# Kernel tuning notes

Hardware: AMD Instinct MI355X
Metric: run time of the kernel (lower is better)

## Reference

```python
import jax, jax.numpy as jnp
import numpy as np
import math

NUM_BITS = 8
EPS = 1e-5


def fake_quant(x, num_bits=NUM_BITS):
    """Uniform fake quantization over the tensor's full range (min/max), STE-friendly."""
    qmax = 2.0 ** num_bits - 1.0
    mn = jnp.min(x)
    mx = jnp.max(x)
    scale = jnp.maximum((mx - mn) / qmax, 1e-8)
    q = jnp.round(jnp.clip((x - mn) / scale, 0.0, qmax)) * scale + mn
    # straight-through estimator: forward = q, backward = identity
    return x + jax.lax.stop_gradient(q - x)


def qconv(x, w, stride, pad):
    """QConv2d: fake-quantize input (8b) and weight (8b), then fp conv (no bias)."""
    return jax.lax.conv_general_dilated(
        fake_quant(x), fake_quant(w),
        window_strides=(stride, stride),
        padding=[(pad, pad), (pad, pad)],
        dimension_numbers=("NCHW", "OIHW", "NCHW"))


def range_norm(x, gamma, beta):
    """RangeN / RangeBN (Banner et al.): per-channel mean subtraction and
    range-based scale (max-min over N,H,W) with the Gaussian range correction
    factor; affine params with 8-bit fake-quantized gamma."""
    B, C, H, W = x.shape
    n = B * H * W  # elements per channel
    scale_fix = (0.5 * 0.35) * (1.0 + (math.pi * math.log(4.0)) ** 0.5) / ((2.0 * math.log(n)) ** 0.5)
    mean = jnp.mean(x, axis=(0, 2, 3), keepdims=True)          # [1,C,1,1]
    xc = x - mean
    rng = jnp.max(xc, axis=(0, 2, 3), keepdims=True) - jnp.min(xc, axis=(0, 2, 3), keepdims=True)
    out = xc / (rng * scale_fix + EPS)
    qg = fake_quant(gamma)
    return out * qg[None, :, None, None] + beta[None, :, None, None]


def qsum(a, b):
    """Qsum: fake-quantize both addends to 8 bits, then add."""
    return fake_quant(a) + fake_quant(b)


def setup_inputs() -> dict:
    key = jax.random.key(0)
    ks = jax.random.split(key, 4)
    B, Cin, H, W = 64, 1024, 14, 14
    P = 256  # planes; expansion 4 -> Cout = 1024 == Cin (identity residual)
    x = jax.random.normal(ks[0], (B, Cin, H, W), jnp.float32)
    w1 = jax.random.normal(ks[1], (P, Cin, 1, 1), jnp.float32) * (1.0 / math.sqrt(Cin))
    w2 = jax.random.normal(ks[2], (P, P, 3, 3), jnp.float32) * (1.0 / math.sqrt(P * 9))
    w3 = jax.random.normal(ks[3], (4 * P, P, 1, 1), jnp.float32) * (1.0 / math.sqrt(P))
    g1 = jnp.ones((P,), jnp.float32); b1 = jnp.zeros((P,), jnp.float32)
    g2 = jnp.ones((P,), jnp.float32); b2 = jnp.zeros((P,), jnp.float32)
    g3 = jnp.ones((4 * P,), jnp.float32); b3 = jnp.zeros((4 * P,), jnp.float32)
    return {"x": x, "w1": w1, "g1": g1, "b1": b1, "w2": w2, "g2": g2, "b2": b2,
            "w3": w3, "g3": g3, "b3": b3}


def reference(x, w1, g1, b1, w2, g2, b2, w3, g3, b3):
    out = qconv(x, w1, stride=1, pad=0)
    out = range_norm(out, g1, b1)
    out = qconv(out, w2, stride=1, pad=1)
    out = range_norm(out, g2, b2)
    out = qconv(out, w3, stride=1, pad=0)
    out = range_norm(out, g3, b3)
    return qsum(x, out)  # downsample is None -> identity residual
```

## Files before the change

### kernel.cpp

```cpp
#include <hip/hip_runtime.h>
#include <math.h>

#ifndef M_PI
#define M_PI 3.14159265358979323846
#endif

#define NB   64
#define NCOL 12544

typedef __attribute__((ext_vector_type(4))) int int4v;

static const size_t OF_OUT = 0;
static const size_t OF_XC  = 3211264;
static const size_t OF_Z1P = 6422528;
static const size_t OF_Z2C = 7471104;
static const size_t OF_WQ1 = 8273920;
static const size_t OF_WQ2 = 8339456;
static const size_t OF_WQ3 = 8486912;
static const size_t OF_R1  = 8552448;
static const size_t OF_R2  = 8552704;
static const size_t OF_R3  = 8552960;
static const size_t OF_T2  = 8553984;
static const size_t OF_CX  = 8556032;
static const size_t OF_U2  = 8568576;
static const size_t OF_V2  = 8584960;
static const size_t OF_CZ  = 8597504;
static const size_t OF_P1  = 8610048;
static const size_t OF_P2  = 8685312;
static const size_t OF_P3  = 8760576;
static const size_t OF_PMM = 9061632;
static const size_t OF_RS  = 9064192;
static const size_t OF_ST  = 9068800;
static const size_t OF_MS  = 9068864;

__device__ __forceinline__ float fqv(float v, float mn, float sc) {
    float t = (v - mn) / sc;
    t = fminf(fmaxf(t, 0.0f), 255.0f);
    return rintf(t) * sc + mn;
}
__device__ __forceinline__ float codef(float v, float mn, float sc) {
    float t = (v - mn) / sc;
    t = fminf(fmaxf(t, 0.0f), 255.0f);
    return rintf(t) - 128.0f;
}
__device__ __forceinline__ unsigned short f2bf(float f) { return (unsigned short)(__float_as_uint(f) >> 16); }
__device__ __forceinline__ float bf2f(unsigned short u) { return __uint_as_float(((unsigned)u) << 16); }
__device__ __forceinline__ int pack4(float a, float b, float c, float d) {
    return (int)(unsigned char)(signed char)(int)a | ((int)(unsigned char)(signed char)(int)b << 8) |
           ((int)(unsigned char)(signed char)(int)c << 16) | ((int)(unsigned char)(signed char)(int)d << 24);
}
__device__ __forceinline__ void glds16(const void* g, void* l) {
    __builtin_amdgcn_global_load_lds((const __attribute__((address_space(1))) unsigned int*)g,
                                     (__attribute__((address_space(3))) unsigned int*)l, 16, 0, 0);
}

__global__ __launch_bounds__(256) void k_minmax_all(const float4* __restrict__ x, const float4* __restrict__ w1,
                                                    const float4* __restrict__ w2, const float4* __restrict__ w3,
                                                    float* __restrict__ Pmm) {
    int b = blockIdx.x;
    const float4* p; int lb, nb, n4, base;
    if (b < 1024)      { p = x;  lb = b;        nb = 1024; n4 = 3211264; base = 0; }
    else if (b < 1088) { p = w1; lb = b - 1024; nb = 64;   n4 = 65536;   base = 2048; }
    else if (b < 1216) { p = w2; lb = b - 1088; nb = 128;  n4 = 147456;  base = 2176; }
    else               { p = w3; lb = b - 1216; nb = 64;   n4 = 65536;   base = 2432; }
    float mn = INFINITY, mx = -INFINITY;
    for (int i = lb * 256 + threadIdx.x; i < n4; i += nb * 256) {
        float4 v = p[i];
        mn = fminf(mn, fminf(fminf(v.x, v.y), fminf(v.z, v.w)));
        mx = fmaxf(mx, fmaxf(fmaxf(v.x, v.y), fmaxf(v.z, v.w)));
    }
    for (int o = 32; o; o >>= 1) {
        mn = fminf(mn, __shfl_down(mn, o, 64));
        mx = fmaxf(mx, __shfl_down(mx, o, 64));
    }
    __shared__ float smn[4], smx[4];
    int lane = threadIdx.x & 63, w = threadIdx.x >> 6;
    if (lane == 0) { smn[w] = mn; smx[w] = mx; }
    __syncthreads();
    if (threadIdx.x == 0) {
        for (int i = 1; i < 4; i++) { mn = fminf(mn, smn[i]); mx = fmaxf(mx, smx[i]); }
        Pmm[base + lb * 2]     = mn;
        Pmm[base + lb * 2 + 1] = mx;
    }
}

__global__ __launch_bounds__(256) void k_fqparams2(const float* __restrict__ Pmm, float* __restrict__ sf) {
    __shared__ float sa[4], sb[4];
    int t = threadIdx.x, lane = t & 63, w = t >> 6;
    const int nbs[4]   = {1024, 64, 128, 64};
    const int bases[4] = {0, 2048, 2176, 2432};
    for (int ten = 0; ten < 4; ten++) {
        float mn = INFINITY, mx = -INFINITY;
        for (int i = t; i < nbs[ten]; i += 256) {
            mn = fminf(mn, Pmm[bases[ten] + 2 * i]);
            mx = fmaxf(mx, Pmm[bases[ten] + 2 * i + 1]);
        }
        for (int o = 32; o; o >>= 1) {
            mn = fminf(mn, __shfl_down(mn, o, 64));
            mx = fmaxf(mx, __shfl_down(mx, o, 64));
        }
        if (lane == 0) { sa[w] = mn; sb[w] = mx; }
        __syncthreads();
        if (t == 0) {
            mn = fminf(fminf(sa[0], sa[1]), fminf(sa[2], sa[3]));
            mx = fmaxf(fmaxf(sb[0], sb[1]), fmaxf(sb[2], sb[3]));
            sf[8 + 3 * ten] = mn;
            sf[9 + 3 * ten] = fmaxf((mx - mn) / 255.0f, 1e-8f);
        }
        __syncthreads();
    }
}

__global__ __launch_bounds__(256) void k_wcode_all(const float* __restrict__ w1, const float* __restrict__ w2,
                                                   const float* __restrict__ w3, const float* __restrict__ sf,
                                                   signed char* __restrict__ wq1, signed char* __restrict__ wq2,
                                                   signed char* __restrict__ wq3,
                                                   float* __restrict__ R1, float* __restrict__ R2,
                                                   float* __restrict__ R3, float* __restrict__ T8) {
    __shared__ float sh[64];
    int b = blockIdx.x, t = threadIdx.x;
    int lane = t & 63, wv = t >> 6;
    if (b < 1280) {
        const float* w; signed char* wc; float* R; int K, co; const float* pw;
        if (b < 256) { w = w1; wc = wq1; R = R1; K = 1024; co = b; pw = sf + 11; }
        else         { w = w3; wc = wq3; R = R3; K = 256;  co = b - 256; pw = sf + 17; }
        float mn = pw[0], s = pw[1];
        float sum = 0.f;
        for (int k0 = t * 4; k0 < K; k0 += 1024) {
            float4 v = *(const float4*)&w[(size_t)co * K + k0];
            float c0 = codef(v.x, mn, s), c1 = codef(v.y, mn, s), c2 = codef(v.z, mn, s), c3 = codef(v.w, mn, s);
            *(int*)&wc[(size_t)co * K + k0] = pack4(c0, c1, c2, c3);
            sum += c0 + c1 + c2 + c3;
        }
        for (int o = 32; o; o >>= 1) sum += __shfl_down(sum, o, 64);
        if (lane == 0) sh[wv] = sum;
        __syncthreads();
        if (t == 0) R[co] = sh[0] + sh[1] + sh[2] + sh[3];
    } else {
        int co = b - 1280, ci = t;
        float mn = sf[14], s = sf[15];
        float tp[9];
#pragma unroll
        for (int p = 0; p < 9; p++) {
            float c = codef(w2[((size_t)co * 256 + ci) * 9 + p], mn, s);
            wq2[(size_t)co * 2304 + p * 256 + ci] = (signed char)(int)c;
            tp[p] = c;
        }
        float* red = sh;
        float* sT = sh + 40;
#pragma unroll
        for (int p = 0; p < 9; p++) {
            float v = tp[p];
            for (int o = 32; o; o >>= 1) v += __shfl_down(v, o, 64);
            if (lane == 0) red[wv * 9 + p] = v;
        }
        __syncthreads();
        if (ci < 9) sT[ci] = red[ci] + red[9 + ci] + red[18 + ci] + red[27 + ci];
        __syncthreads();
        if (ci == 0) {
            float T0 = sT[0], T1 = sT[1], T2 = sT[2], T3 = sT[3],
                  T5 = sT[5], T6 = sT[6], T7 = sT[7], T8v = sT[8];
            R2[co] = T0 + T1 + T2 + T3 + sT[4] + T5 + T6 + T7 + T8v;
            float* o = &T8[co * 8];
            o[0] = T0 + T1 + T2;
            o[1] = T6 + T7 + T8v;
            o[2] = T0 + T3 + T6;
            o[3] = T2 + T5 + T8v;
            o[4] = T0; o[5] = T2; o[6] = T6; o[7] = T8v;
        }
    }
}

__global__ __launch_bounds__(256) void k_code0(const float* __restrict__ x, signed char* __restrict__ dst,
                                               const float* __restrict__ qp, float* __restrict__ CX) {
    __shared__ unsigned short lt[28][264];
    int n = blockIdx.z, hw0 = blockIdx.x * 28, cq = blockIdx.y * 256;
    int t = threadIdx.x;
    float qmn = qp[0], qsc = qp[1];
    const float* sp = x + ((size_t)n * 1024 + cq) * 196 + hw0;
    for (int i = t; i < 7168; i += 256) {
        int c = i / 28, hw = i - c * 28;
        lt[hw][c] = f2bf(codef(sp[(size_t)c * 196 + hw], qmn, qsc));
    }
    __syncthreads();
    int lane = t & 63, wv = t >> 6;
    int c0 = lane * 4;
#pragma unroll
    for (int s = 0; s < 7; s++) {
        int i = s * 4 + wv;
        int pk = pack4(bf2f(lt[i][c0]), bf2f(lt[i][c0 + 1]), bf2f(lt[i][c0 + 2]), bf2f(lt[i][c0 + 3]));
        *(int*)&dst[((size_t)n * 196 + hw0 + i) * 1024 + cq + c0] = pk;
    }
    for (int i = wv; i < 28; i += 4) {
        float s = bf2f(lt[i][lane]) + bf2f(lt[i][lane + 64]) +
                  bf2f(lt[i][lane + 128]) + bf2f(lt[i][lane + 192]);
        for (int o = 32; o; o >>= 1) s += __shfl_down(s, o, 64);
        if (lane == 0) atomicAdd(&CX[n * 196 + hw0 + i], s);
    }
}

template <int PAD>
__global__ __launch_bounds__(256) void k_codeE(const float* __restrict__ src, signed char* __restrict__ dst,
                                               const float* __restrict__ mean, const float* __restrict__ sg,
                                               const float* __restrict__ beta, const float* __restrict__ qp,
                                               float* __restrict__ rowsum) {
    int t = threadIdx.x, lane = t & 63, wv = t >> 6;
    int c4 = lane * 4;
    float4 m4 = *(const float4*)&mean[c4];
    float4 s4 = *(const float4*)&sg[c4];
    float4 b4 = *(const float4*)&beta[c4];
    float qmn = qp[0], qsc = qp[1];
#pragma unroll
    for (int r = 0; r < 4; r++) {
        int j = blockIdx.x * 16 + wv * 4 + r;
        float4 v = *(const float4*)&src[(size_t)j * 256 + c4];
        float c0 = codef((v.x - m4.x) * s4.x + b4.x, qmn, qsc);
        float c1 = codef((v.y - m4.y) * s4.y + b4.y, qmn, qsc);
        float c2 = codef((v.z - m4.z) * s4.z + b4.z, qmn, qsc);
        float c3 = codef((v.w - m4.w) * s4.w + b4.w, qmn, qsc);
        int n = j / 196, hw = j - n * 196, h = hw / 14, w = hw - (hw / 14) * 14;
        size_t di;
        if (PAD) di = (((size_t)n * 16 + h + 1) * 16 + (w + 1)) * 256 + c4;
        else     di = (size_t)j * 256 + c4;
        *(int*)&dst[di] = pack4(c0, c1, c2, c3);
        float s = c0 + c1 + c2 + c3;
        for (int o = 32; o; o >>= 1) s += __shfl_down(s, o, 64);
        if (lane == 0) {
            if (PAD) rowsum[((size_t)n * 16 + h + 1) * 16 + (w + 1)] = s;
            else     rowsum[j] = s;
        }
    }
}

__global__ __launch_bounds__(256) void k_v2(const float* __restrict__ U, float* __restrict__ V) {
    int j = blockIdx.x * 256 + threadIdx.x;
    if (j >= NCOL) return;
    int n = j / 196, hw = j - n * 196, h = hw / 14, w = hw - (hw / 14) * 14;
    const float* u = U + (size_t)n * 256;
    float s = 0.f;
#pragma unroll
    for (int r = 0; r < 3; r++)
#pragma unroll
        for (int c = 0; c < 3; c++) s += u[(h + r) * 16 + (w + c)];
    V[j] = s;
}

template <int MODE>
__global__ __launch_bounds__(256, 2) void k_conv12(const signed char* __restrict__ Acts,
                                                   const signed char* __restrict__ Wts,
                                                   const float* __restrict__ R, const float* __restrict__ T8,
                                                   const float* __restrict__ Cj,
                                                   const float* __restrict__ pw, const float* __restrict__ pz,
                                                   float* __restrict__ outNHWC, int K,
                                                   float* __restrict__ Ps, float* __restrict__ Pn,
                                                   float* __restrict__ Px) {
    __shared__ __align__(16) signed char As[2 * 16384];
    __shared__ __align__(16) signed char Bs[2 * 8192];
    __shared__ float Lst[2][64][3];
    int tid = threadIdx.x, lane = tid & 63, wave = tid >> 6;
    int wm = wave >> 1, wn = wave & 1;
    int jb = blockIdx.x * 128, cob = blockIdx.y * 64;
    int sr = tid >> 3, spos = tid & 7, sc = spos ^ (sr & 7);

    const signed char* aq[4];
#pragma unroll
    for (int q = 0; q < 4; q++) {
        int j = jb + q * 32 + sr;
        if (MODE == 0) aq[q] = Acts + (size_t)j * K + sc * 16;
        else {
            int n = j / 196, hw = j - n * 196, h = hw / 14, w = hw - (hw / 14) * 14;
            aq[q] = Acts + (((size_t)n * 16 + h) * 16 + w) * 256 + sc * 16;
        }
    }
    const signed char* bq[2];
#pragma unroll
    for (int q = 0; q < 2; q++) bq[q] = Wts + (size_t)(cob + q * 32 + sr) * K + sc * 16;

    int4v acc[4][2];
#pragma unroll
    for (int mi = 0; mi < 4; mi++)
#pragma unroll
        for (int ni = 0; ni < 2; ni++) acc[mi][ni] = (int4v)0;

    int nk = K >> 7;
    auto stage = [&](int b, int ks) {
        size_t koA;
        if (MODE == 0) koA = (size_t)ks << 7;
        else {
            int k = ks << 7;
            int p = k >> 8, kin = k & 255;
            int rr = p / 3, ss = p - 3 * rr;
            koA = (size_t)(rr * 16 + ss) * 256 + kin;
        }
#pragma unroll
        for (int q = 0; q < 4; q++)
            glds16(aq[q] + koA, &As[b * 16384 + (q * 32 + sr) * 128 + spos * 16]);
#pragma unroll
        for (int q = 0; q < 2; q++)
            glds16(bq[q] + ((size_t)ks << 7), &Bs[b * 8192 + (q * 32 + sr) * 128 + spos * 16]);
    };

    int l15 = lane & 15, kq = lane >> 4, sw = l15 & 7;
    stage(0, 0);
    for (int ks = 0; ks < nk; ks++) {
        __syncthreads();
        if (ks + 1 < nk) stage((ks + 1) & 1, ks + 1);
        int b = ks & 1;
#pragma unroll
        for (int kc = 0; kc < 2; kc++) {
            int col = ((kc * 4 + kq) ^ sw) << 4;
            int4v a[4], bb[2];
#pragma unroll
            for (int mi = 0; mi < 4; mi++)
                a[mi] = *(const int4v*)&As[b * 16384 + (wm * 64 + mi * 16 + l15) * 128 + col];
#pragma unroll
            for (int ni = 0; ni < 2; ni++)
                bb[ni] = *(const int4v*)&Bs[b * 8192 + (wn * 32 + ni * 16 + l15) * 128 + col];
#pragma unroll
            for (int mi = 0; mi < 4; mi++)
#pragma unroll
                for (int ni = 0; ni < 2; ni++)
                    acc[mi][ni] = __builtin_amdgcn_mfma_i32_16x16x64_i8(a[mi], bb[ni], acc[mi][ni], 0, 0, 0);
        }
    }

    float aw = pw[1], bw = pw[0] + 128.f * pw[1];
    float az = pz[1], bz = pz[0] + 128.f * pz[1];
    float caa = aw * az, cR = aw * bz, cC = bw * az, cK = bw * bz;
    int cco[2]; float rr0[2]; float t8v[2][8];
#pragma unroll
    for (int ni = 0; ni < 2; ni++) {
        cco[ni] = cob + wn * 32 + ni * 16 + l15;
        rr0[ni] = R[cco[ni]];
        if (MODE == 1) {
#pragma unroll
            for (int p = 0; p < 8; p++) t8v[ni][p] = T8[cco[ni] * 8 + p];
        }
    }
    float ssm[2] = {0.f, 0.f}, smnv[2] = {INFINITY, INFINITY}, smxv[2] = {-INFINITY, -INFINITY};
#pragma unroll
    for (int mi = 0; mi < 4; mi++)
#pragma unroll
        for (int reg = 0; reg < 4; reg++) {
            int j = jb + wm * 64 + mi * 16 + kq * 4 + reg;
            int n = j / 196, hw = j - n * 196;
            float cj = Cj[j];
            float constterm;
            float pt = 0.f, pb = 0.f, pl = 0.f, pr = 0.f, ctl = 0.f, ctr = 0.f, cbl = 0.f, cbr = 0.f;
            if (MODE == 1) {
                int h = hw / 14, w = hw - (hw / 14) * 14;
                pt = (h == 0) ? 1.f : 0.f;  pb = (h == 13) ? 1.f : 0.f;
                pl = (w == 0) ? 1.f : 0.f;  pr = (w == 13) ? 1.f : 0.f;
                ctl = pt * pl; ctr = pt * pr; cbl = pb * pl; cbr = pb * pr;
                float miss = 3.f * (pt + pb + pl + pr) - (ctl + ctr + cbl + cbr);
                constterm = cK * (256.f * (9.f - miss));
            } else {
                constterm = cK * (float)K;
            }
#pragma unroll
            for (int ni = 0; ni < 2; ni++) {
                float rsum = rr0[ni];
                if (MODE == 1)
                    rsum -= pt * t8v[ni][0] + pb * t8v[ni][1] + pl * t8v[ni][2] + pr * t8v[ni][3]
                          - ctl * t8v[ni][4] - ctr * t8v[ni][5] - cbl * t8v[ni][6] - cbr * t8v[ni][7];
                float v = caa * (float)acc[mi][ni][reg] + cR * rsum + cC * cj + constterm;
                outNHWC[(size_t)j * 256 + cco[ni]] = v;
                ssm[ni] += v;
                smnv[ni] = fminf(smnv[ni], v);
                smxv[ni] = fmaxf(smxv[ni], v);
            }
        }
#pragma unroll
    for (int ni = 0; ni < 2; ni++) {
        float s = ssm[ni], mn = smnv[ni], mx = smxv[ni];
        s += __shfl_xor(s, 16, 64); s += __shfl_xor(s, 32, 64);
        mn = fminf(mn, __shfl_xor(mn, 16, 64)); mn = fminf(mn, __shfl_xor(mn, 32, 64));
        mx = fmaxf(mx, __shfl_xor(mx, 16, 64)); mx = fmaxf(mx, __shfl_xor(mx, 32, 64));
        if (kq == 0) {
            int cl = wn * 32 + ni * 16 + l15;
            Lst[wm][cl][0] = s; Lst[wm][cl][1] = mn; Lst[wm][cl][2] = mx;
        }
    }
    __syncthreads();
    if (tid < 64) {
        float s  = Lst[0][tid][0] + Lst[1][tid][0];
        float mn = fminf(Lst[0][tid][1], Lst[1][tid][1]);
        float mx = fmaxf(Lst[0][tid][2], Lst[1][tid][2]);
        int idx = blockIdx.x * 256 + cob + tid;
        Ps[idx] = s; Pn[idx] = mn; Px[idx] = mx;
    }
}

__global__ __launch_bounds__(256, 2) void k_conv3(const signed char* __restrict__ Wts,
                                                  const signed char* __restrict__ Zc,
                                                  const float* __restrict__ R, const float* __restrict__ Cj,
                                                  const float* __restrict__ pw, const float* __restrict__ pz,
                                                  float* __restrict__ out,
                                                  float* __restrict__ Ps, float* __restrict__ Pn,
                                                  float* __restrict__ Px) {
    __shared__ __align__(16) signed char As[32768];
    __shared__ __align__(16) signed char Bs[32768];
    __shared__ float Lst[2][128][3];
    int tid = threadIdx.x, lane = tid & 63, wave = tid >> 6;
    int wm = wave >> 1, wn = wave & 1;
    int jb = blockIdx.x * 128, cob = blockIdx.y * 128;
    int sr = tid >> 4, spos = tid & 15;
#pragma unroll
    for (int p = 0; p < 8; p++) {
        int row = p * 16 + sr;
        int cg = spos ^ (row & 7);
        glds16(Zc + (size_t)(jb + row) * 256 + cg * 16, &As[p * 4096 + tid * 16]);
    }
#pragma unroll
    for (int p = 0; p < 8; p++) {
        int row = p * 16 + sr;
        int cg = spos ^ (row & 7);
        glds16(Wts + (size_t)(cob + row) * 256 + cg * 16, &Bs[p * 4096 + tid * 16]);
    }
    __syncthreads();

    int4v acc[4][4];
#pragma unroll
    for (int mi = 0; mi < 4; mi++)
#pragma unroll
        for (int ni = 0; ni < 4; ni++) acc[mi][ni] = (int4v)0;

    int l15 = lane & 15, kq = lane >> 4, sw = l15 & 7;
#pragma unroll
    for (int kc = 0; kc < 4; kc++) {
        int col = ((kc * 4 + kq) ^ sw) << 4;
        int4v a[4], bb[4];
#pragma unroll
        for (int mi = 0; mi < 4; mi++)
            a[mi] = *(const int4v*)&As[(wm * 64 + mi * 16 + l15) * 256 + col];
#pragma unroll
        for (int ni = 0; ni < 4; ni++)
            bb[ni] = *(const int4v*)&Bs[(wn * 64 + ni * 16 + l15) * 256 + col];
#pragma unroll
        for (int mi = 0; mi < 4; mi++)
#pragma unroll
            for (int ni = 0; ni < 4; ni++)
                acc[mi][ni] = __builtin_amdgcn_mfma_i32_16x16x64_i8(a[mi], bb[ni], acc[mi][ni], 0, 0, 0);
    }

    float aw = pw[1], bw = pw[0] + 128.f * pw[1];
    float az = pz[1], bz = pz[0] + 128.f * pz[1];
    float caa = aw * az, cR = aw * bz, cC = bw * az, cK = bw * bz;
    int coA[4]; float rA[4];
#pragma unroll
    for (int ni = 0; ni < 4; ni++) {
        coA[ni] = cob + wn * 64 + ni * 16 + l15;
        rA[ni] = R[coA[ni]];
    }
    float ps[4], pmn[4], pmx[4];
#pragma unroll
    for (int ni = 0; ni < 4; ni++) { ps[ni] = 0.f; pmn[ni] = INFINITY; pmx[ni] = -INFINITY; }
#pragma unroll
    for (int mi = 0; mi < 4; mi++) {
        int j0 = jb + wm * 64 + mi * 16 + kq * 4;
        int n = j0 / 196, hh = j0 - n * 196;
        float4 cj = *(const float4*)&Cj[j0];
#pragma unroll
        for (int ni = 0; ni < 4; ni++) {
            float base = cR * rA[ni] + cK * 256.f;
            float4 v;
            v.x = caa * (float)acc[mi][ni][0] + base + cC * cj.x;
            v.y = caa * (float)acc[mi][ni][1] + base + cC * cj.y;
            v.z = caa * (float)acc[mi][ni][2] + base + cC * cj.z;
            v.w = caa * (float)acc[mi][ni][3] + base + cC * cj.w;
            *(float4*)&out[((size_t)n * 1024 + coA[ni]) * 196 + hh] = v;
            ps[ni] += v.x + v.y + v.z + v.w;
            pmn[ni] = fminf(pmn[ni], fminf(fminf(v.x, v.y), fminf(v.z, v.w)));
            pmx[ni] = fmaxf(pmx[ni], fmaxf(fmaxf(v.x, v.y), fmaxf(v.z, v.w)));
        }
    }
#pragma unroll
    for (int ni = 0; ni < 4; ni++) {
        float s = ps[ni], mn = pmn[ni], mx = pmx[ni];
        s += __shfl_xor(s, 16, 64); s += __shfl_xor(s, 32, 64);
        mn = fminf(mn, __shfl_xor(mn, 16, 64)); mn = fminf(mn, __shfl_xor(mn, 32, 64));
        mx = fmaxf(mx, __shfl_xor(mx, 16, 64)); mx = fmaxf(mx, __shfl_xor(mx, 32, 64));
        if (kq == 0) {
            int cl = wn * 64 + ni * 16 + l15;
            Lst[wm][cl][0] = s; Lst[wm][cl][1] = mn; Lst[wm][cl][2] = mx;
        }
    }
    __syncthreads();
    if (tid < 128) {
        float s  = Lst[0][tid][0] + Lst[1][tid][0];
        float mn = fminf(Lst[0][tid][1], Lst[1][tid][1]);
        float mx = fmaxf(Lst[0][tid][2], Lst[1][tid][2]);
        int idx = blockIdx.x * 1024 + cob + tid;
        Ps[idx] = s; Pn[idx] = mn; Px[idx] = mx;
    }
}

__global__ __launch_bounds__(256) void k_redstats(const float* __restrict__ Ps, const float* __restrict__ Pn,
                                                  const float* __restrict__ Px, int C,
                                                  float* __restrict__ sum_o, float* __restrict__ mn_o,
                                                  float* __restrict__ mx_o) {
    __shared__ float Ls[4][64][3];
    int t = threadIdx.x, cl = t & 63, sl = t >> 6;
    int co = blockIdx.x * 64 + cl;
    float s = 0.f, mn = INFINITY, mx = -INFINITY;
    for (int b = sl; b < 98; b += 4) {
        s += Ps[b * C + co];
        mn = fminf(mn, Pn[b * C + co]);
        mx = fmaxf(mx, Px[b * C + co]);
    }
    Ls[sl][cl][0] = s; Ls[sl][cl][1] = mn; Ls[sl][cl][2] = mx;
    __syncthreads();
    if (t < 64) {
        s = Ls[0][t][0] + Ls[1][t][0] + Ls[2][t][0] + Ls[3][t][0];
        mn = fminf(fminf(Ls[0][t][1], Ls[1][t][1]), fminf(Ls[2][t][1], Ls[3][t][1]));
        mx = fmaxf(fmaxf(Ls[0][t][2], Ls[1][t][2]), fmaxf(Ls[2][t][2], Ls[3][t][2]));
        int co2 = blockIdx.x * 64 + t;
        sum_o[co2] = s; mn_o[co2] = mn; mx_o[co2] = mx;
    }
}

__global__ __launch_bounds__(256) void k_finnorm(int C, const float* __restrict__ gamma, const float* __restrict__ beta,
                                                 const float* __restrict__ sum_i, const float* __restrict__ mn_i,
                                                 const float* __restrict__ mx_i, float* mean_o, float* sg_o,
                                                 float* qp, float scale_fix) {
    int tid = threadIdx.x;
    int lane = tid & 63, w = tid >> 6;
    __shared__ float sa[4], sb[4];
    float gmn = INFINITY, gmx = -INFINITY;
    for (int c = tid; c < C; c += 256) { float g = gamma[c]; gmn = fminf(gmn, g); gmx = fmaxf(gmx, g); }
    for (int o = 32; o; o >>= 1) { gmn = fminf(gmn, __shfl_down(gmn, o, 64)); gmx = fmaxf(gmx, __shfl_down(gmx, o, 64)); }
    if (lane == 0) { sa[w] = gmn; sb[w] = gmx; }
    __syncthreads();
    gmn = fminf(fminf(sa[0], sa[1]), fminf(sa[2], sa[3]));
    gmx = fmaxf(fmaxf(sb[0], sb[1]), fmaxf(sb[2], sb[3]));
    float gsc = fmaxf((gmx - gmn) / 255.0f, 1e-8f);
    __syncthreads();
    float qmn = INFINITY, qmx = -INFINITY;
    for (int c = tid; c < C; c += 256) {
        float mean = sum_i[c] / 12544.0f;
        float cmn = mn_i[c], cmx = mx_i[c];
        float rng = cmx - cmn;
        float qg = fqv(gamma[c], gmn, gsc);
        float s = qg / (rng * scale_fix + 1e-5f);
        mean_o[c] = mean; sg_o[c] = s;
        float b = beta[c];
        float lo = (cmn - mean) * s + b;
        float hi = (cmx - mean) * s + b;
        qmn = fminf(qmn, fminf(lo, hi));
        qmx = fmaxf(qmx, fmaxf(lo, hi));
    }
    for (int o = 32; o; o >>= 1) { qmn = fminf(qmn, __shfl_down(qmn, o, 64)); qmx = fmaxf(qmx, __shfl_down(qmx, o, 64)); }
    if (lane == 0) { sa[w] = qmn; sb[w] = qmx; }
    __syncthreads();
    if (tid == 0) {
        qmn = fminf(fminf(sa[0], sa[1]), fminf(sa[2], sa[3]));
        qmx = fmaxf(fmaxf(sb[0], sb[1]), fmaxf(sb[2], sb[3]));
        qp[0] = qmn;
        qp[1] = fmaxf((qmx - qmn) / 255.0f, 1e-8f);
    }
}

__global__ __launch_bounds__(256) void k_final(const float* __restrict__ x, float* __restrict__ out,
                                               const float* __restrict__ mean, const float* __restrict__ sg,
                                               const float* __restrict__ beta, const float* __restrict__ sf,
                                               const float* __restrict__ qp) {
    float xmn = sf[8], xsc = sf[9];
    float qmn = qp[0], qsc = qp[1];
    const float4* xp = (const float4*)x;
    float4* yp = (float4*)out;
    int n4 = 12845056 / 4;
    int i = blockIdx.x * blockDim.x + threadIdx.x;
    int str = gridDim.x * blockDim.x;
    for (; i < n4; i += str) {
        int e = i * 4;
        int c = (e / 196) & 1023;
        float m = mean[c], s = sg[c], b = beta[c];
        float4 xv = xp[i], ov = yp[i], r;
        r.x = fqv(xv.x, xmn, xsc) + fqv((ov.x - m) * s + b, qmn, qsc);
        r.y = fqv(xv.y, xmn, xsc) + fqv((ov.y - m) * s + b, qmn, qsc);
        r.z = fqv(xv.z, xmn, xsc) + fqv((ov.z - m) * s + b, qmn, qsc);
        r.w = fqv(xv.w, xmn, xsc) + fqv((ov.w - m) * s + b, qmn, qsc);
        yp[i] = r;
    }
}

extern "C" void kernel_launch(void* const* d_in, const int* in_sizes, int n_in,
                              void* d_out, int out_size, void* d_ws, size_t ws_size,
                              hipStream_t stream) {
    const float* x  = (const float*)d_in[0];
    const float* w1 = (const float*)d_in[1];
    const float* g1 = (const float*)d_in[2];
    const float* b1 = (const float*)d_in[3];
    const float* w2 = (const float*)d_in[4];
    const float* g2 = (const float*)d_in[5];
    const float* b2 = (const float*)d_in[6];
    const float* w3 = (const float*)d_in[7];
    const float* g3 = (const float*)d_in[8];
    const float* b3 = (const float*)d_in[9];
    float* out = (float*)d_out;

    float* W = (float*)d_ws;
    float* OUT = W + OF_OUT;
    signed char* xc  = (signed char*)(W + OF_XC);
    signed char* z1p = (signed char*)(W + OF_Z1P);
    signed char* z2c = (signed char*)(W + OF_Z2C);
    signed char* wq1 = (signed char*)(W + OF_WQ1);
    signed char* wq2 = (signed char*)(W + OF_WQ2);
    signed char* wq3 = (signed char*)(W + OF_WQ3);
    float* R1 = W + OF_R1; float* R2 = W + OF_R2; float* R3 = W + OF_R3;
    float* T2 = W + OF_T2;
    float* CX = W + OF_CX; float* U2 = W + OF_U2; float* V2 = W + OF_V2; float* CZ = W + OF_CZ;
    float* P1s = W + OF_P1, *P1n = P1s + 25088, *P1x = P1s + 50176;
    float* P2s = W + OF_P2, *P2n = P2s + 25088, *P2x = P2s + 50176;
    float* P3s = W + OF_P3, *P3n = P3s + 100352, *P3x = P3s + 200704;
    float* Pmm = W + OF_PMM;
    float* RS = W + OF_RS;
    float* sum1 = RS, *mn1 = RS + 256, *mx1 = RS + 512;
    float* sum2 = RS + 768, *mn2 = RS + 1024, *mx2 = RS + 1280;
    float* sum3 = RS + 1536, *mn3 = RS + 2560, *mx3 = RS + 3584;
    float* S = W + OF_ST;
    float* MS = W + OF_MS;
    float* mean1 = MS, *sg1 = MS + 256, *mean2 = MS + 512, *sg2 = MS + 768, *mean3 = MS + 1024, *sg3 = MS + 2048;

    const float scale_fix =
        (float)((0.5 * 0.35) * (1.0 + sqrt(M_PI * log(4.0))) / sqrt(2.0 * log(12544.0)));

    hipMemsetAsync(CX, 0, 12544 * 4, stream);
    hipMemsetAsync(U2, 0, 16384 * 4, stream);
    hipMemsetAsync(z1p, 0, 4194304, stream);

    k_minmax_all<<<1280, 256, 0, stream>>>((const float4*)x, (const float4*)w1,
                                           (const float4*)w2, (const float4*)w3, Pmm);
    k_fqparams2<<<1, 256, 0, stream>>>(Pmm, S);

    k_wcode_all<<<1536, 256, 0, stream>>>(w1, w2, w3, S, wq1, wq2, wq3, R1, R2, R3, T2);

    k_code0<<<dim3(7, 4, 64), 256, 0, stream>>>(x, xc, S + 8, CX);

    k_conv12<0><<<dim3(98, 4), 256, 0, stream>>>(xc, wq1, R1, nullptr, CX, S + 11, S + 8, OUT, 1024,
                                                 P1s, P1n, P1x);
    k_redstats<<<4, 256, 0, stream>>>(P1s, P1n, P1x, 256, sum1, mn1, mx1);
    k_finnorm<<<1, 256, 0, stream>>>(256, g1, b1, sum1, mn1, mx1, mean1, sg1, S + 20, scale_fix);
    k_codeE<1><<<784, 256, 0, stream>>>(OUT, z1p, mean1, sg1, b1, S + 20, U2);
    k_v2<<<49, 256, 0, stream>>>(U2, V2);

    k_conv12<1><<<dim3(98, 4), 256, 0, stream>>>(z1p, wq2, R2, T2, V2, S + 14, S + 20, OUT, 2304,
                                                 P2s, P2n, P2x);
    k_redstats<<<4, 256, 0, stream>>>(P2s, P2n, P2x, 256, sum2, mn2, mx2);
    k_finnorm<<<1, 256, 0, stream>>>(256, g2, b2, sum2, mn2, mx2, mean2, sg2, S + 23, scale_fix);
    k_codeE<0><<<784, 256, 0, stream>>>(OUT, z2c, mean2, sg2, b2, S + 23, CZ);

    k_conv3<<<dim3(98, 8), 256, 0, stream>>>(wq3, z2c, R3, CZ, S + 17, S + 23, out, P3s, P3n, P3x);
    k_redstats<<<16, 256, 0, stream>>>(P3s, P3n, P3x, 1024, sum3, mn3, mx3);
    k_finnorm<<<1, 256, 0, stream>>>(1024, g3, b3, sum3, mn3, mx3, mean3, sg3, S + 26, scale_fix);
    k_final<<<2048, 256, 0, stream>>>(x, out, mean3, sg3, b3, S, S + 26);
}
```

Before: 282.1 us.

## Shrink conv tiles, drop atomics/memsets, and fuse stats reduction kernels

Halves the M tile of conv1/conv2 and the N tile of conv3, doubling grid size and raising launch-bound occupancy so more blocks run concurrently across CUs. Replaces the atomic column-sum in the input coding pass with per-slice partial buffers summed in the conv epilogue, removing two memsets. The v2 halo sum now reads an unpadded rowsum with bounds checks, and the separate redstats/finnorm kernels are merged into one 1024-thread kernel, cutting launches. Smaller tiles reduce data reuse per block and increase partial-stat traffic.

```diff
diff --git a/kernel.cpp b/kernel.cpp
--- a/kernel.cpp
+++ b/kernel.cpp
@@ -21,17 +21,16 @@
 static const size_t OF_R2  = 8552704;
 static const size_t OF_R3  = 8552960;
 static const size_t OF_T2  = 8553984;
-static const size_t OF_CX  = 8556032;
-static const size_t OF_U2  = 8568576;
-static const size_t OF_V2  = 8584960;
-static const size_t OF_CZ  = 8597504;
-static const size_t OF_P1  = 8610048;
-static const size_t OF_P2  = 8685312;
-static const size_t OF_P3  = 8760576;
-static const size_t OF_PMM = 9061632;
-static const size_t OF_RS  = 9064192;
-static const size_t OF_ST  = 9068800;
-static const size_t OF_MS  = 9068864;
+static const size_t OF_CXP = 8556032;
+static const size_t OF_U2  = 8606208;
+static const size_t OF_V2  = 8618752;
+static const size_t OF_CZ  = 8631296;
+static const size_t OF_P1  = 8643840;
+static const size_t OF_P2  = 8794368;
+static const size_t OF_P3  = 8944896;
+static const size_t OF_PMM = 9245952;
+static const size_t OF_ST  = 9248512;
+static const size_t OF_MS  = 9248576;
 
 __device__ __forceinline__ float fqv(float v, float mn, float sc) {
     float t = (v - mn) / sc;
@@ -172,7 +171,7 @@
 }
 
 __global__ __launch_bounds__(256) void k_code0(const float* __restrict__ x, signed char* __restrict__ dst,
-                                               const float* __restrict__ qp, float* __restrict__ CX) {
+                                               const float* __restrict__ qp, float* __restrict__ CXp) {
     __shared__ unsigned short lt[28][264];
     int n = blockIdx.z, hw0 = blockIdx.x * 28, cq = blockIdx.y * 256;
     int t = threadIdx.x;
@@ -195,7 +194,7 @@
         float s = bf2f(lt[i][lane]) + bf2f(lt[i][lane + 64]) +
                   bf2f(lt[i][lane + 128]) + bf2f(lt[i][lane + 192]);
         for (int o = 32; o; o >>= 1) s += __shfl_down(s, o, 64);
-        if (lane == 0) atomicAdd(&CX[n * 196 + hw0 + i], s);
+        if (lane == 0) CXp[blockIdx.y * NCOL + n * 196 + hw0 + i] = s;
     }
 }
 
@@ -218,17 +217,15 @@
         float c1 = codef((v.y - m4.y) * s4.y + b4.y, qmn, qsc);
         float c2 = codef((v.z - m4.z) * s4.z + b4.z, qmn, qsc);
         float c3 = codef((v.w - m4.w) * s4.w + b4.w, qmn, qsc);
-        int n = j / 196, hw = j - n * 196, h = hw / 14, w = hw - (hw / 14) * 14;
         size_t di;
-        if (PAD) di = (((size_t)n * 16 + h + 1) * 16 + (w + 1)) * 256 + c4;
-        else     di = (size_t)j * 256 + c4;
+        if (PAD) {
+            int n = j / 196, hw = j - n * 196, h = hw / 14, w = hw - (hw / 14) * 14;
+            di = (((size_t)n * 16 + h + 1) * 16 + (w + 1)) * 256 + c4;
+        } else di = (size_t)j * 256 + c4;
         *(int*)&dst[di] = pack4(c0, c1, c2, c3);
         float s = c0 + c1 + c2 + c3;
         for (int o = 32; o; o >>= 1) s += __shfl_down(s, o, 64);
-        if (lane == 0) {
-            if (PAD) rowsum[((size_t)n * 16 + h + 1) * 16 + (w + 1)] = s;
-            else     rowsum[j] = s;
-        }
+        if (lane == 0) rowsum[j] = s;
     }
 }
 
@@ -236,17 +233,24 @@
     int j = blockIdx.x * 256 + threadIdx.x;
     if (j >= NCOL) return;
     int n = j / 196, hw = j - n * 196, h = hw / 14, w = hw - (hw / 14) * 14;
-    const float* u = U + (size_t)n * 256;
+    const float* u = U + (size_t)n * 196;
     float s = 0.f;
 #pragma unroll
-    for (int r = 0; r < 3; r++)
-#pragma unroll
-        for (int c = 0; c < 3; c++) s += u[(h + r) * 16 + (w + c)];
+    for (int dh = -1; dh <= 1; dh++) {
+        int hh = h + dh;
+        if (hh < 0 || hh >= 14) continue;
+#pragma unroll
+        for (int dw = -1; dw <= 1; dw++) {
+            int ww = w + dw;
+            if (ww < 0 || ww >= 14) continue;
+            s += u[hh * 14 + ww];
+        }
+    }
     V[j] = s;
 }
 
 template <int MODE>
-__global__ __launch_bounds__(256, 2) void k_conv12(const signed char* __restrict__ Acts,
+__global__ __launch_bounds__(256, 4) void k_conv12(const signed char* __restrict__ Acts,
                                                    const signed char* __restrict__ Wts,
                                                    const float* __restrict__ R, const float* __restrict__ T8,
                                                    const float* __restrict__ Cj,
@@ -254,17 +258,17 @@
                                                    float* __restrict__ outNHWC, int K,
                                                    float* __restrict__ Ps, float* __restrict__ Pn,
                                                    float* __restrict__ Px) {
-    __shared__ __align__(16) signed char As[2 * 16384];
+    __shared__ __align__(16) signed char As[2 * 8192];
     __shared__ __align__(16) signed char Bs[2 * 8192];
     __shared__ float Lst[2][64][3];
     int tid = threadIdx.x, lane = tid & 63, wave = tid >> 6;
     int wm = wave >> 1, wn = wave & 1;
-    int jb = blockIdx.x * 128, cob = blockIdx.y * 64;
+    int jb = blockIdx.x * 64, cob = blockIdx.y * 64;
     int sr = tid >> 3, spos = tid & 7, sc = spos ^ (sr & 7);
 
-    const signed char* aq[4];
-#pragma unroll
-    for (int q = 0; q < 4; q++) {
+    const signed char* aq[2];
+#pragma unroll
+    for (int q = 0; q < 2; q++) {
         int j = jb + q * 32 + sr;
         if (MODE == 0) aq[q] = Acts + (size_t)j * K + sc * 16;
         else {
@@ -276,9 +280,9 @@
 #pragma unroll
     for (int q = 0; q < 2; q++) bq[q] = Wts + (size_t)(cob + q * 32 + sr) * K + sc * 16;
 
-    int4v acc[4][2];
-#pragma unroll
-    for (int mi = 0; mi < 4; mi++)
+    int4v acc[2][2];
+#pragma unroll
+    for (int mi = 0; mi < 2; mi++)
 #pragma unroll
         for (int ni = 0; ni < 2; ni++) acc[mi][ni] = (int4v)0;
 
@@ -293,8 +297,8 @@
             koA = (size_t)(rr * 16 + ss) * 256 + kin;
         }
 #pragma unroll
-        for (int q = 0; q < 4; q++)
-            glds16(aq[q] + koA, &As[b * 16384 + (q * 32 + sr) * 128 + spos * 16]);
+        for (int q = 0; q < 2; q++)
+            glds16(aq[q] + koA, &As[b * 8192 + (q * 32 + sr) * 128 + spos * 16]);
 #pragma unroll
         for (int q = 0; q < 2; q++)
             glds16(bq[q] + ((size_t)ks << 7), &Bs[b * 8192 + (q * 32 + sr) * 128 + spos * 16]);
@@ -309,15 +313,15 @@
 #pragma unroll
         for (int kc = 0; kc < 2; kc++) {
             int col = ((kc * 4 + kq) ^ sw) << 4;
-            int4v a[4], bb[2];
-#pragma unroll
-            for (int mi = 0; mi < 4; mi++)
-                a[mi] = *(const int4v*)&As[b * 16384 + (wm * 64 + mi * 16 + l15) * 128 + col];
+            int4v a[2], bb[2];
+#pragma unroll
+            for (int mi = 0; mi < 2; mi++)
+                a[mi] = *(const int4v*)&As[b * 8192 + (wm * 32 + mi * 16 + l15) * 128 + col];
 #pragma unroll
             for (int ni = 0; ni < 2; ni++)
                 bb[ni] = *(const int4v*)&Bs[b * 8192 + (wn * 32 + ni * 16 + l15) * 128 + col];
 #pragma unroll
-            for (int mi = 0; mi < 4; mi++)
+            for (int mi = 0; mi < 2; mi++)
 #pragma unroll
                 for (int ni = 0; ni < 2; ni++)
                     acc[mi][ni] = __builtin_amdgcn_mfma_i32_16x16x64_i8(a[mi], bb[ni], acc[mi][ni], 0, 0, 0);
@@ -339,15 +343,17 @@
     }
     float ssm[2] = {0.f, 0.f}, smnv[2] = {INFINITY, INFINITY}, smxv[2] = {-INFINITY, -INFINITY};
 #pragma unroll
-    for (int mi = 0; mi < 4; mi++)
+    for (int mi = 0; mi < 2; mi++)
 #pragma unroll
         for (int reg = 0; reg < 4; reg++) {
-            int j = jb + wm * 64 + mi * 16 + kq * 4 + reg;
-            int n = j / 196, hw = j - n * 196;
-            float cj = Cj[j];
+            int j = jb + wm * 32 + mi * 16 + kq * 4 + reg;
+            float cj;
+            if (MODE == 0) cj = Cj[j] + Cj[NCOL + j] + Cj[2 * NCOL + j] + Cj[3 * NCOL + j];
+            else cj = Cj[j];
             float constterm;
             float pt = 0.f, pb = 0.f, pl = 0.f, pr = 0.f, ctl = 0.f, ctr = 0.f, cbl = 0.f, cbr = 0.f;
             if (MODE == 1) {
+                int hw = j - (j / 196) * 196;
                 int h = hw / 14, w = hw - (hw / 14) * 14;
                 pt = (h == 0) ? 1.f : 0.f;  pb = (h == 13) ? 1.f : 0.f;
                 pl = (w == 0) ? 1.f : 0.f;  pr = (w == 13) ? 1.f : 0.f;
@@ -391,7 +397,7 @@
     }
 }
 
-__global__ __launch_bounds__(256, 2) void k_conv3(const signed char* __restrict__ Wts,
+__global__ __launch_bounds__(256, 3) void k_conv3(const signed char* __restrict__ Wts,
                                                   const signed char* __restrict__ Zc,
                                                   const float* __restrict__ R, const float* __restrict__ Cj,
                                                   const float* __restrict__ pw, const float* __restrict__ pz,
@@ -399,69 +405,67 @@
                                                   float* __restrict__ Ps, float* __restrict__ Pn,
                                                   float* __restrict__ Px) {
     __shared__ __align__(16) signed char As[32768];
-    __shared__ __align__(16) signed char Bs[32768];
-    __shared__ float Lst[2][128][3];
+    __shared__ __align__(16) signed char Bs[16384];
+    __shared__ float Lst[2][64][3];
     int tid = threadIdx.x, lane = tid & 63, wave = tid >> 6;
     int wm = wave >> 1, wn = wave & 1;
-    int jb = blockIdx.x * 128, cob = blockIdx.y * 128;
+    int jb = blockIdx.x * 128, cob = blockIdx.y * 64;
     int sr = tid >> 4, spos = tid & 15;
 #pragma unroll
     for (int p = 0; p < 8; p++) {
         int row = p * 16 + sr;
         int cg = spos ^ (row & 7);
-        glds16(Zc + (size_t)(jb + row) * 256 + cg * 16, &As[p * 4096 + tid * 16]);
-    }
-#pragma unroll
-    for (int p = 0; p < 8; p++) {
+        glds16(Zc + (size_t)(jb + row) * 256 + cg * 16, &As[row * 256 + spos * 16]);
+    }
+#pragma unroll
+    for (int p = 0; p < 4; p++) {
         int row = p * 16 + sr;
         int cg = spos ^ (row & 7);
-        glds16(Wts + (size_t)(cob + row) * 256 + cg * 16, &Bs[p * 4096 + tid * 16]);
-    }
-    __syncthreads();
-
-    int4v acc[4][4];
+        glds16(Wts + (size_t)(cob + row) * 256 + cg * 16, &Bs[row * 256 + spos * 16]);
+    }
+    __syncthreads();
+
+    int4v acc[4][2];
 #pragma unroll
     for (int mi = 0; mi < 4; mi++)
 #pragma unroll
-        for (int ni = 0; ni < 4; ni++) acc[mi][ni] = (int4v)0;
+        for (int ni = 0; ni < 2; ni++) acc[mi][ni] = (int4v)0;
 
     int l15 = lane & 15, kq = lane >> 4, sw = l15 & 7;
 #pragma unroll
     for (int kc = 0; kc < 4; kc++) {
         int col = ((kc * 4 + kq) ^ sw) << 4;
-        int4v a[4], bb[4];
+        int4v a[4], bb[2];
 #pragma unroll
         for (int mi = 0; mi < 4; mi++)
             a[mi] = *(const int4v*)&As[(wm * 64 + mi * 16 + l15) * 256 + col];
 #pragma unroll
-        for (int ni = 0; ni < 4; ni++)
-            bb[ni] = *(const int4v*)&Bs[(wn * 64 + ni * 16 + l15) * 256 + col];
+        for (int ni = 0; ni < 2; ni++)
+            bb[ni] = *(const int4v*)&Bs[(wn * 32 + ni * 16 + l15) * 256 + col];
 #pragma unroll
         for (int mi = 0; mi < 4; mi++)
 #pragma unroll
-            for (int ni = 0; ni < 4; ni++)
+            for (int ni = 0; ni < 2; ni++)
                 acc[mi][ni] = __builtin_amdgcn_mfma_i32_16x16x64_i8(a[mi], bb[ni], acc[mi][ni], 0, 0, 0);
     }
 
     float aw = pw[1], bw = pw[0] + 128.f * pw[1];
     float az = pz[1], bz = pz[0] + 128.f * pz[1];
     float caa = aw * az, cR = aw * bz, cC = bw * az, cK = bw * bz;
-    int coA[4]; float rA[4];
-#pragma unroll
-    for (int ni = 0; ni < 4; ni++) {
-        coA[ni] = cob + wn * 64 + ni * 16 + l15;
+    int coA[2]; float rA[2];
+#pragma unroll
+    for (int ni = 0; ni < 2; ni++) {
+        coA[ni] = cob + wn * 32 + ni * 16 + l15;
         rA[ni] = R[coA[ni]];
     }
-    float ps[4], pmn[4], pmx[4];
-#pragma unroll
-    for (int ni = 0; ni < 4; ni++) { ps[ni] = 0.f; pmn[ni] = INFINITY; pmx[ni] = -INFINITY; }
+    float ps[2] = {0.f, 0.f}, pmn[2] = {INFINITY, INFINITY}, pmx[2] = {-INFINITY, -INFINITY};
 #pragma unroll
     for (int mi = 0; mi < 4; mi++) {
         int j0 = jb + wm * 64 + mi * 16 + kq * 4;
         int n = j0 / 196, hh = j0 - n * 196;
         float4 cj = *(const float4*)&Cj[j0];
 #pragma unroll
-        for (int ni = 0; ni < 4; ni++) {
+        for (int ni = 0; ni < 2; ni++) {
             float base = cR * rA[ni] + cK * 256.f;
             float4 v;
             v.x = caa * (float)acc[mi][ni][0] + base + cC * cj.x;
@@ -475,18 +479,18 @@
         }
     }
 #pragma unroll
-    for (int ni = 0; ni < 4; ni++) {
+    for (int ni = 0; ni < 2; ni++) {
         float s = ps[ni], mn = pmn[ni], mx = pmx[ni];
         s += __shfl_xor(s, 16, 64); s += __shfl_xor(s, 32, 64);
         mn = fminf(mn, __shfl_xor(mn, 16, 64)); mn = fminf(mn, __shfl_xor(mn, 32, 64));
         mx = fmaxf(mx, __shfl_xor(mx, 16, 64)); mx = fmaxf(mx, __shfl_xor(mx, 32, 64));
         if (kq == 0) {
-            int cl = wn * 64 + ni * 16 + l15;
+            int cl = wn * 32 + ni * 16 + l15;
             Lst[wm][cl][0] = s; Lst[wm][cl][1] = mn; Lst[wm][cl][2] = mx;
         }
     }
     __syncthreads();
-    if (tid < 128) {
+    if (tid < 64) {
         float s  = Lst[0][tid][0] + Lst[1][tid][0];
         float mn = fminf(Lst[0][tid][1], Lst[1][tid][1]);
         float mx = fmaxf(Lst[0][tid][2], Lst[1][tid][2]);
@@ -495,68 +499,63 @@
     }
 }
 
-__global__ __launch_bounds__(256) void k_redstats(const float* __restrict__ Ps, const float* __restrict__ Pn,
-                                                  const float* __restrict__ Px, int C,
-                                                  float* __restrict__ sum_o, float* __restrict__ mn_o,
-                                                  float* __restrict__ mx_o) {
-    __shared__ float Ls[4][64][3];
-    int t = threadIdx.x, cl = t & 63, sl = t >> 6;
-    int co = blockIdx.x * 64 + cl;
+__global__ __launch_bounds__(1024) void k_finstats(int C, int NP,
+                                                   const float* __restrict__ gamma, const float* __restrict__ beta,
+                                                   const float* __restrict__ Ps, const float* __restrict__ Pn,
+                                                   const float* __restrict__ Px,
+                                                   float* __restrict__ mean_o, float* __restrict__ sg_o,
+                                                   float* __restrict__ qp, float scale_fix) {
+    __shared__ float Ss[1024], Sn[1024], Sx[1024];
+    __shared__ float wr1[16], wr2[16];
+    int t = threadIdx.x, lane = t & 63, wv = t >> 6;
+    int c, sl, stride;
+    if (C == 256) { c = t & 255; sl = t >> 8; stride = 4; }
+    else          { c = t;       sl = 0;      stride = 1; }
     float s = 0.f, mn = INFINITY, mx = -INFINITY;
-    for (int b = sl; b < 98; b += 4) {
-        s += Ps[b * C + co];
-        mn = fminf(mn, Pn[b * C + co]);
-        mx = fmaxf(mx, Px[b * C + co]);
-    }
-    Ls[sl][cl][0] = s; Ls[sl][cl][1] = mn; Ls[sl][cl][2] = mx;
-    __syncthreads();
-    if (t < 64) {
-        s = Ls[0][t][0] + Ls[1][t][0] + Ls[2][t][0] + Ls[3][t][0];
-        mn = fminf(fminf(Ls[0][t][1], Ls[1][t][1]), fminf(Ls[2][t][1], Ls[3][t][1]));
-        mx = fmaxf(fmaxf(Ls[0][t][2], Ls[1][t][2]), fmaxf(Ls[2][t][2], Ls[3][t][2]));
-        int co2 = blockIdx.x * 64 + t;
-        sum_o[co2] = s; mn_o[co2] = mn; mx_o[co2] = mx;
-    }
-}
-
-__global__ __launch_bounds__(256) void k_finnorm(int C, const float* __restrict__ gamma, const float* __restrict__ beta,
-                                                 const float* __restrict__ sum_i, const float* __restrict__ mn_i,
-                                                 const float* __restrict__ mx_i, float* mean_o, float* sg_o,
-                                                 float* qp, float scale_fix) {
-    int tid = threadIdx.x;
-    int lane = tid & 63, w = tid >> 6;
-    __shared__ float sa[4], sb[4];
-    float gmn = INFINITY, gmx = -INFINITY;
-    for (int c = tid; c < C; c += 256) { float g = gamma[c]; gmn = fminf(gmn, g); gmx = fmaxf(gmx, g); }
+    for (int b = sl; b < NP; b += stride) {
+        int idx = b * C + c;
+        s += Ps[idx]; mn = fminf(mn, Pn[idx]); mx = fmaxf(mx, Px[idx]);
+    }
+    Ss[t] = s; Sn[t] = mn; Sx[t] = mx;
+    __syncthreads();
+    float gv = (t < C) ? gamma[t] : gamma[0];
+    float gmn = gv, gmx = gv;
     for (int o = 32; o; o >>= 1) { gmn = fminf(gmn, __shfl_down(gmn, o, 64)); gmx = fmaxf(gmx, __shfl_down(gmx, o, 64)); }
-    if (lane == 0) { sa[w] = gmn; sb[w] = gmx; }
-    __syncthreads();
-    gmn = fminf(fminf(sa[0], sa[1]), fminf(sa[2], sa[3]));
-    gmx = fmaxf(fmaxf(sb[0], sb[1]), fmaxf(sb[2], sb[3]));
+    if (lane == 0) { wr1[wv] = gmn; wr2[wv] = gmx; }
+    __syncthreads();
+    if (t == 0) {
+        float a = wr1[0], b2 = wr2[0];
+        for (int i = 1; i < 16; i++) { a = fminf(a, wr1[i]); b2 = fmaxf(b2, wr2[i]); }
+        wr1[0] = a; wr2[0] = b2;
+    }
+    __syncthreads();
+    gmn = wr1[0]; gmx = wr2[0];
     float gsc = fmaxf((gmx - gmn) / 255.0f, 1e-8f);
-    __syncthreads();
     float qmn = INFINITY, qmx = -INFINITY;
-    for (int c = tid; c < C; c += 256) {
-        float mean = sum_i[c] / 12544.0f;
-        float cmn = mn_i[c], cmx = mx_i[c];
-        float rng = cmx - cmn;
-        float qg = fqv(gamma[c], gmn, gsc);
-        float s = qg / (rng * scale_fix + 1e-5f);
-        mean_o[c] = mean; sg_o[c] = s;
-        float b = beta[c];
-        float lo = (cmn - mean) * s + b;
-        float hi = (cmx - mean) * s + b;
-        qmn = fminf(qmn, fminf(lo, hi));
-        qmx = fmaxf(qmx, fmaxf(lo, hi));
-    }
+    if (t < C) {
+        if (C == 256) {
+            s  = Ss[t] + Ss[t + 256] + Ss[t + 512] + Ss[t + 768];
+            mn = fminf(fminf(Sn[t], Sn[t + 256]), fminf(Sn[t + 512], Sn[t + 768]));
+            mx = fmaxf(fmaxf(Sx[t], Sx[t + 256]), fmaxf(Sx[t + 512], Sx[t + 768]));
+        } else { s = Ss[t]; mn = Sn[t]; mx = Sx[t]; }
+        float mean = s / 12544.0f;
+        float rng = mx - mn;
+        float qg = fqv(gamma[t], gmn, gsc);
+        float sg = qg / (rng * scale_fix + 1e-5f);
+        mean_o[t] = mean; sg_o[t] = sg;
+        float b3 = beta[t];
+        float lo = (mn - mean) * sg + b3, hi = (mx - mean) * sg + b3;
+        qmn = fminf(lo, hi); qmx = fmaxf(lo, hi);
+    }
+    __syncthreads();
     for (int o = 32; o; o >>= 1) { qmn = fminf(qmn, __shfl_down(qmn, o, 64)); qmx = fmaxf(qmx, __shfl_down(qmx, o, 64)); }
-    if (lane == 0) { sa[w] = qmn; sb[w] = qmx; }
-    __syncthreads();
-    if (tid == 0) {
-        qmn = fminf(fminf(sa[0], sa[1]), fminf(sa[2], sa[3]));
-        qmx = fmaxf(fmaxf(sb[0], sb[1]), fmaxf(sb[2], sb[3]));
-        qp[0] = qmn;
-        qp[1] = fmaxf((qmx - qmn) / 255.0f, 1e-8f);
+    if (lane == 0) { wr1[wv] = qmn; wr2[wv] = qmx; }
+    __syncthreads();
+    if (t == 0) {
+        float a = INFINITY, b2 = -INFINITY;
+        for (int i = 0; i < 16; i++) { a = fminf(a, wr1[i]); b2 = fmaxf(b2, wr2[i]); }
+        qp[0] = a;
+        qp[1] = fmaxf((b2 - a) / 255.0f, 1e-8f);
     }
 }
 
@@ -609,15 +608,11 @@
     signed char* wq3 = (signed char*)(W + OF_WQ3);
     float* R1 = W + OF_R1; float* R2 = W + OF_R2; float* R3 = W + OF_R3;
     float* T2 = W + OF_T2;
-    float* CX = W + OF_CX; float* U2 = W + OF_U2; float* V2 = W + OF_V2; float* CZ = W + OF_CZ;
-    float* P1s = W + OF_P1, *P1n = P1s + 25088, *P1x = P1s + 50176;
-    float* P2s = W + OF_P2, *P2n = P2s + 25088, *P2x = P2s + 50176;
+    float* CXp = W + OF_CXP; float* U2 = W + OF_U2; float* V2 = W + OF_V2; float* CZ = W + OF_CZ;
+    float* P1s = W + OF_P1, *P1n = P1s + 50176, *P1x = P1s + 100352;
+    float* P2s = W + OF_P2, *P2n = P2s + 50176, *P2x = P2s + 100352;
     float* P3s = W + OF_P3, *P3n = P3s + 100352, *P3x = P3s + 200704;
     float* Pmm = W + OF_PMM;
-    float* RS = W + OF_RS;
-    float* sum1 = RS, *mn1 = RS + 256, *mx1 = RS + 512;
-    float* sum2 = RS + 768, *mn2 = RS + 1024, *mx2 = RS + 1280;
-    float* sum3 = RS + 1536, *mn3 = RS + 2560, *mx3 = RS + 3584;
     float* S = W + OF_ST;
     float* MS = W + OF_MS;
     float* mean1 = MS, *sg1 = MS + 256, *mean2 = MS + 512, *sg2 = MS + 768, *mean3 = MS + 1024, *sg3 = MS + 2048;
@@ -625,8 +620,6 @@
     const float scale_fix =
         (float)((0.5 * 0.35) * (1.0 + sqrt(M_PI * log(4.0))) / sqrt(2.0 * log(12544.0)));
 
-    hipMemsetAsync(CX, 0, 12544 * 4, stream);
-    hipMemsetAsync(U2, 0, 16384 * 4, stream);
     hipMemsetAsync(z1p, 0, 4194304, stream);
 
     k_minmax_all<<<1280, 256, 0, stream>>>((const float4*)x, (const float4*)w1,
@@ -635,23 +628,20 @@
 
     k_wcode_all<<<1536, 256, 0, stream>>>(w1, w2, w3, S, wq1, wq2, wq3, R1, R2, R3, T2);
 
-    k_code0<<<dim3(7, 4, 64), 256, 0, stream>>>(x, xc, S + 8, CX);
-
-    k_conv12<0><<<dim3(98, 4), 256, 0, stream>>>(xc, wq1, R1, nullptr, CX, S + 11, S + 8, OUT, 1024,
-                                                 P1s, P1n, P1x);
-    k_redstats<<<4, 256, 0, stream>>>(P1s, P1n, P1x, 256, sum1, mn1, mx1);
-    k_finnorm<<<1, 256, 0, stream>>>(256, g1, b1, sum1, mn1, mx1, mean1, sg1, S + 20, scale_fix);
+    k_code0<<<dim3(7, 4, 64), 256, 0, stream>>>(x, xc, S + 8, CXp);
+
+    k_conv12<0><<<dim3(196, 4), 256, 0, stream>>>(xc, wq1, R1, nullptr, CXp, S + 11, S + 8, OUT, 1024,
+                                                  P1s, P1n, P1x);
+    k_finstats<<<1, 1024, 0, stream>>>(256, 196, g1, b1, P1s, P1n, P1x, mean1, sg1, S + 20, scale_fix);
     k_codeE<1><<<784, 256, 0, stream>>>(OUT, z1p, mean1, sg1, b1, S + 20, U2);
     k_v2<<<49, 256, 0, stream>>>(U2, V2);
 
-    k_conv12<1><<<dim3(98, 4), 256, 0, stream>>>(z1p, wq2, R2, T2, V2, S + 14, S + 20, OUT, 2304,
-                                                 P2s, P2n, P2x);
-    k_redstats<<<4, 256, 0, stream>>>(P2s, P2n, P2x, 256, sum2, mn2, mx2);
-    k_finnorm<<<1, 256, 0, stream>>>(256, g2, b2, sum2, mn2, mx2, mean2, sg2, S + 23, scale_fix);
+    k_conv12<1><<<dim3(196, 4), 256, 0, stream>>>(z1p, wq2, R2, T2, V2, S + 14, S + 20, OUT, 2304,
+                                                  P2s, P2n, P2x);
+    k_finstats<<<1, 1024, 0, stream>>>(256, 196, g2, b2, P2s, P2n, P2x, mean2, sg2, S + 23, scale_fix);
     k_codeE<0><<<784, 256, 0, stream>>>(OUT, z2c, mean2, sg2, b2, S + 23, CZ);
 
-    k_conv3<<<dim3(98, 8), 256, 0, stream>>>(wq3, z2c, R3, CZ, S + 17, S + 23, out, P3s, P3n, P3x);
-    k_redstats<<<16, 256, 0, stream>>>(P3s, P3n, P3x, 1024, sum3, mn3, mx3);
-    k_finnorm<<<1, 256, 0, stream>>>(1024, g3, b3, sum3, mn3, mx3, mean3, sg3, S + 26, scale_fix);
+    k_conv3<<<dim3(98, 16), 256, 0, stream>>>(wq3, z2c, R3, CZ, S + 17, S + 23, out, P3s, P3n, P3x);
+    k_finstats<<<1, 1024, 0, stream>>>(1024, 98, g3, b3, P3s, P3n, P3x, mean3, sg3, S + 26, scale_fix);
     k_final<<<2048, 256, 0, stream>>>(x, out, mean3, sg3, b3, S, S + 26);
 }
```

Measured after the change: 312.2 us. 10.7% more time.
